# Kernel tuning notes

Hardware: AMD Instinct MI355X
Metric: run time of the kernel (lower is better)

## Reference

```python
import jax, jax.numpy as jnp
import numpy as np

# Faithful translations of the torch lambdas:
# r0: identity; r90: transpose(-2,-1); r180: flip(-2); r270: transpose(-2,-1) then flip(-1)
_r0 = lambda xi: xi
_r90 = lambda xi: jnp.swapaxes(xi, -2, -1)
_r180 = lambda xi: jnp.flip(xi, axis=-2)
_r270 = lambda xi: jnp.flip(jnp.swapaxes(xi, -2, -1), axis=-1)


def setup_inputs() -> dict:
    key = jax.random.key(0)
    kx, kl = jax.random.split(key)
    B, C, H, W = 256, 3, 224, 224  # square spatial required by transpose-in-place semantics
    x = jax.random.normal(kx, (B, C, H, W), dtype=jnp.float32)
    label = jax.random.randint(kl, (B,), 0, 4, dtype=jnp.int32)
    return {"x": x, "label": label}


def reference(x, label):
    # Single fused per-sample-indexed rotation via vmap + lax.switch —
    # replaces the python loop / per-sample kernel launches of the original.
    def rotate_one(xi, li):
        return jax.lax.switch(li, [_r0, _r90, _r180, _r270], xi)

    out = jax.vmap(rotate_one)(x, label)
    return (out, label)
```

## Files before the change

kernel.cpp:

```cpp
#include <hip/hip_runtime.h>


#define HW 224
#define TILE 32
#define NT 7

__global__ __launch_bounds__(256) void rot4_kernel(const float* __restrict__ x,
                                                   const int* __restrict__ label,
                                                   float* __restrict__ out) {
    int tile = blockIdx.x;
    int tw = tile % NT; tile /= NT;
    int th = tile % NT; tile /= NT;
    int c  = tile % 3;  tile /= 3;
    int b  = tile;

    const int lab = label[b];
    const size_t plane = (size_t)(b * 3 + c) * (HW * HW);
    const float* __restrict__ in = x + plane;
    float* __restrict__ o = out + plane;

    const int h0 = th * TILE;
    const int w0 = tw * TILE;

    const int t  = threadIdx.x;
    const int r  = t >> 3;
    const int c4 = t & 7;

    if (lab == 0 || lab == 2) {
        const int in_row = (lab == 0) ? (h0 + r) : (HW - 1 - (h0 + r));
        float4 v = *(const float4*)(in + (size_t)in_row * HW + w0 + c4 * 4);
        *(float4*)(o + (size_t)(h0 + r) * HW + w0 + c4 * 4) = v;
    } else {
        __shared__ float tb[TILE][TILE + 1];
        const int rbase = (lab == 1) ? w0 : (HW - TILE - w0);
        float4 v = *(const float4*)(in + (size_t)(rbase + r) * HW + h0 + c4 * 4);
        tb[r][c4 * 4 + 0] = v.x;
        tb[r][c4 * 4 + 1] = v.y;
        tb[r][c4 * 4 + 2] = v.z;
        tb[r][c4 * 4 + 3] = v.w;
        __syncthreads();
        float4 w;
        if (lab == 1) {
            w.x = tb[c4 * 4 + 0][r];
            w.y = tb[c4 * 4 + 1][r];
            w.z = tb[c4 * 4 + 2][r];
            w.w = tb[c4 * 4 + 3][r];
        } else {
            w.x = tb[31 - (c4 * 4 + 0)][r];
            w.y = tb[31 - (c4 * 4 + 1)][r];
            w.z = tb[31 - (c4 * 4 + 2)][r];
            w.w = tb[31 - (c4 * 4 + 3)][r];
        }
        *(float4*)(o + (size_t)(h0 + r) * HW + w0 + c4 * 4) = w;
    }
}

__global__ void label_kernel(const int* __restrict__ label, float* __restrict__ out, int n) {
    int i = blockIdx.x * blockDim.x + threadIdx.x;
    if (i < n) out[i] = (float)label[i];
}

extern "C" void kernel_launch(void* const* d_in, const int* in_sizes, int n_in,
                              void* d_out, int out_size, void* d_ws, size_t ws_size,
                              hipStream_t stream) {
    const float* x     = (const float*)d_in[0];
    const int*   label = (const int*)d_in[1];
    float*       out   = (float*)d_out;

    const int B = in_sizes[1];
    const int nblocks = B * 3 * NT * NT;

    rot4_kernel<<<nblocks, 256, 0, stream>>>(x, label, out);

    const size_t img_elems = (size_t)B * 3 * HW * HW;
    label_kernel<<<(B + 255) / 256, 256, 0, stream>>>(label, out + img_elems, B);
}
```

Before: 261.7 us.

## Process full 32-row strips per block with nontemporal accesses and fused label copy

Each block now handles a whole 32x224 strip, so the grid is seven times smaller, and it loops over the seven tiles. Rotations by 90 and 270 degrees use a double-buffered shared-memory transpose that prefetches the next tile's load before the barrier. Identity and flip paths become contiguous vectorized copies, and all global traffic uses nontemporal loads and stores. The separate label conversion kernel is folded into the first blocks to remove one launch. The cost is fewer blocks and less parallelism per wave, in exchange for lower per-block overhead and better streaming.

After: 254.3 us. 2.9% less time.

```diff
diff --git a/kernel.cpp b/kernel.cpp
--- a/kernel.cpp
+++ b/kernel.cpp
@@ -2,62 +2,95 @@
 
 
 #define HW 224
+#define W4 56
 #define TILE 32
 #define NT 7
 
+typedef float f4 __attribute__((ext_vector_type(4)));
+
 __global__ __launch_bounds__(256) void rot4_kernel(const float* __restrict__ x,
                                                    const int* __restrict__ label,
-                                                   float* __restrict__ out) {
-    int tile = blockIdx.x;
-    int tw = tile % NT; tile /= NT;
-    int th = tile % NT; tile /= NT;
-    int c  = tile % 3;  tile /= 3;
-    int b  = tile;
+                                                   float* __restrict__ out,
+                                                   float* __restrict__ out_label,
+                                                   int B) {
+    const int t = threadIdx.x;
+
+    {
+        int li = blockIdx.x * 256 + t;
+        if (blockIdx.x < (B + 255) / 256 && li < B) out_label[li] = (float)label[li];
+    }
+
+    int blk = blockIdx.x;
+    const int th = blk % NT; blk /= NT;
+    const int c  = blk % 3;  blk /= 3;
+    const int b  = blk;
 
     const int lab = label[b];
     const size_t plane = (size_t)(b * 3 + c) * (HW * HW);
-    const float* __restrict__ in = x + plane;
-    float* __restrict__ o = out + plane;
+    const float*  in = x + plane;
+    float*        o  = out + plane;
+    const f4* in4 = (const f4*)in;
+    f4*       o4  = (f4*)o;
+    const int h0 = th * TILE;
 
-    const int h0 = th * TILE;
-    const int w0 = tw * TILE;
+    if (lab == 0) {
+        const size_t base = (size_t)h0 * W4;
+        #pragma unroll
+        for (int k = 0; k < NT; ++k) {
+            size_t i = base + (size_t)k * 256 + t;
+            f4 v = __builtin_nontemporal_load(in4 + i);
+            __builtin_nontemporal_store(v, o4 + i);
+        }
+    } else if (lab == 2) {
+        #pragma unroll
+        for (int k = 0; k < NT; ++k) {
+            int idx = k * 256 + t;
+            int rr  = idx / W4;
+            int cc  = idx - rr * W4;
+            size_t src = (size_t)(HW - 1 - (h0 + rr)) * W4 + cc;
+            size_t dst = (size_t)(h0 + rr) * W4 + cc;
+            f4 v = __builtin_nontemporal_load(in4 + src);
+            __builtin_nontemporal_store(v, o4 + dst);
+        }
+    } else {
+        __shared__ float tb[2][TILE][TILE + 1];
+        const int r  = t >> 3;
+        const int c4 = t & 7;
 
-    const int t  = threadIdx.x;
-    const int r  = t >> 3;
-    const int c4 = t & 7;
+        auto src_ptr = [&](int tw) {
+            const int w0 = tw * TILE;
+            const int rbase = (lab == 1) ? w0 : (HW - TILE - w0);
+            return (const f4*)(in + (size_t)(rbase + r) * HW + h0 + c4 * 4);
+        };
 
-    if (lab == 0 || lab == 2) {
-        const int in_row = (lab == 0) ? (h0 + r) : (HW - 1 - (h0 + r));
-        float4 v = *(const float4*)(in + (size_t)in_row * HW + w0 + c4 * 4);
-        *(float4*)(o + (size_t)(h0 + r) * HW + w0 + c4 * 4) = v;
-    } else {
-        __shared__ float tb[TILE][TILE + 1];
-        const int rbase = (lab == 1) ? w0 : (HW - TILE - w0);
-        float4 v = *(const float4*)(in + (size_t)(rbase + r) * HW + h0 + c4 * 4);
-        tb[r][c4 * 4 + 0] = v.x;
-        tb[r][c4 * 4 + 1] = v.y;
-        tb[r][c4 * 4 + 2] = v.z;
-        tb[r][c4 * 4 + 3] = v.w;
-        __syncthreads();
-        float4 w;
-        if (lab == 1) {
-            w.x = tb[c4 * 4 + 0][r];
-            w.y = tb[c4 * 4 + 1][r];
-            w.z = tb[c4 * 4 + 2][r];
-            w.w = tb[c4 * 4 + 3][r];
-        } else {
-            w.x = tb[31 - (c4 * 4 + 0)][r];
-            w.y = tb[31 - (c4 * 4 + 1)][r];
-            w.z = tb[31 - (c4 * 4 + 2)][r];
-            w.w = tb[31 - (c4 * 4 + 3)][r];
+        f4 v = __builtin_nontemporal_load(src_ptr(0));
+        #pragma unroll
+        for (int tw = 0; tw < NT; ++tw) {
+            float (*tbuf)[TILE + 1] = tb[tw & 1];
+            tbuf[r][c4 * 4 + 0] = v.x;
+            tbuf[r][c4 * 4 + 1] = v.y;
+            tbuf[r][c4 * 4 + 2] = v.z;
+            tbuf[r][c4 * 4 + 3] = v.w;
+            if (tw + 1 < NT)
+                v = __builtin_nontemporal_load(src_ptr(tw + 1));
+            __syncthreads();
+            f4 w;
+            if (lab == 1) {
+                w.x = tbuf[c4 * 4 + 0][r];
+                w.y = tbuf[c4 * 4 + 1][r];
+                w.z = tbuf[c4 * 4 + 2][r];
+                w.w = tbuf[c4 * 4 + 3][r];
+            } else {
+                w.x = tbuf[31 - (c4 * 4 + 0)][r];
+                w.y = tbuf[31 - (c4 * 4 + 1)][r];
+                w.z = tbuf[31 - (c4 * 4 + 2)][r];
+                w.w = tbuf[31 - (c4 * 4 + 3)][r];
+            }
+            const int w0 = tw * TILE;
+            __builtin_nontemporal_store(
+                w, (f4*)(o + (size_t)(h0 + r) * HW + w0 + c4 * 4));
         }
-        *(float4*)(o + (size_t)(h0 + r) * HW + w0 + c4 * 4) = w;
     }
-}
-
-__global__ void label_kernel(const int* __restrict__ label, float* __restrict__ out, int n) {
-    int i = blockIdx.x * blockDim.x + threadIdx.x;
-    if (i < n) out[i] = (float)label[i];
 }
 
 extern "C" void kernel_launch(void* const* d_in, const int* in_sizes, int n_in,
@@ -68,10 +101,8 @@
     float*       out   = (float*)d_out;
 
     const int B = in_sizes[1];
-    const int nblocks = B * 3 * NT * NT;
+    const int nblocks = B * 3 * NT;
+    const size_t img_elems = (size_t)B * 3 * HW * HW;
 
-    rot4_kernel<<<nblocks, 256, 0, stream>>>(x, label, out);
-
-    const size_t img_elems = (size_t)B * 3 * HW * HW;
-    label_kernel<<<(B + 255) / 256, 256, 0, stream>>>(label, out + img_elems, B);
+    rot4_kernel<<<nblocks, 256, 0, stream>>>(x, label, out, out + img_elems, B);
 }
```
